# Kernel optimization log

Hardware: AMD Instinct MI355X
Metric: run time of the kernel (lower is better)

Reference implementation:

```python
import jax, jax.numpy as jnp
import numpy as np

RADIUS = [3, 3, 4, 4]
DILATION = [1, 2, 1, 2]
N_HEAD = 4
D_K = 8
SCALE = 1.0 / np.sqrt(8.0)  # module hardcodes sqrt(8)


def _patches(a, r, d):
    # a: (b, t, c, h, w) -> (b, t, c, ls2, h, w), dilated (2r+1)x(2r+1) window,
    # zero padding (invalid positions masked separately).
    b, t, c, h, w = a.shape
    p = r * d
    ap = jnp.pad(a, ((0, 0), (0, 0), (0, 0), (p, p), (p, p)))
    ls = 2 * r + 1
    sl = [ap[..., dy * d:dy * d + h, dx * d:dx * d + w]
          for dy in range(ls) for dx in range(ls)]
    return jnp.stack(sl, axis=3)


def _valid_mask(h, w, r, d):
    # (ls2, h, w) bool: True where window position is inside the image
    m = _patches(jnp.ones((1, 1, 1, h, w)), r, d)
    return m[0, 0, 0] > 0.5


def _head_attn(q, k, v, r, d):
    # q,k,v: (b, t, c, h, w); attention over all t' frames x local window
    b, t, c, h, w = q.shape
    kp = _patches(k, r, d)        # (b, t', c, p, h, w)
    vp = _patches(v, r, d)
    valid = _valid_mask(h, w, r, d)  # (p, h, w)
    e = jnp.einsum('btchw,bscphw->btsphw', q, kp) * SCALE
    e = jnp.where(valid[None, None, None], e, -jnp.inf)  # OOB -> -inf like CUDA kernel
    e = e.reshape(b, t, t * valid.shape[0], h, w)
    attn = jax.nn.softmax(e, axis=2).reshape(b, t, t, -1, h, w)
    return jnp.einsum('btsphw,bscphw->btchw', attn, vp)


def setup_inputs() -> dict:
    key = jax.random.key(0)
    kx, kq, kk, kv, ko = jax.random.split(key, 5)
    C = 32
    std = 1.0 / np.sqrt(C)
    x = jax.random.normal(kx, (2, 5, C, 64, 64), dtype=jnp.float32)
    Wq = jax.random.normal(kq, (N_HEAD * D_K, C), dtype=jnp.float32) * std
    Wk = jax.random.normal(kk, (N_HEAD * D_K, C), dtype=jnp.float32) * std
    Wv = jax.random.normal(kv, (N_HEAD * D_K, C), dtype=jnp.float32) * std
    Wo = jax.random.normal(ko, (C, C), dtype=jnp.float32) * std
    return {"x": x, "Wq": Wq, "Wk": Wk, "Wv": Wv, "Wo": Wo}


def reference(x, Wq, Wk, Wv, Wo):
    # 1x1x1 Conv3d == per-pixel channel matmul
    q = jnp.einsum('btchw,kc->btkhw', x, Wq)
    k = jnp.einsum('btchw,kc->btkhw', x, Wk)
    v = jnp.einsum('btchw,kc->btkhw', x, Wv)
    outs = []
    for i in range(N_HEAD):
        s = slice(i * D_K, (i + 1) * D_K)
        outs.append(_head_attn(q[:, :, s], k[:, :, s], v[:, :, s],
                               RADIUS[i], DILATION[i]))
    out = jnp.concatenate(outs, axis=2)
    out = jnp.einsum('btchw,kc->btkhw', out, Wo)
    return out + x
```

## Files before the change

kernel.cpp:

```cpp
#include <hip/hip_runtime.h>
#include <stdint.h>

#define NT 5
#define NC 32
#define NH 4
#define HW 4096
#define NPIX 40960
#define QS 0.51006972789f
#define EBIAS 12.0f
#define NINF (-__builtin_inff())

typedef _Float16 half_t;
typedef half_t h2 __attribute__((ext_vector_type(2)));

static __device__ __forceinline__ h2 as_h2(uint32_t u) {
  union { uint32_t u; h2 h; } c; c.u = u; return c.h;
}
static __device__ __forceinline__ uint32_t pack_h2(float a, float b) {
  union { h2 h; uint32_t u; } c;
  c.h.x = (half_t)a; c.h.y = (half_t)b;
  return c.u;
}

#if __has_builtin(__builtin_amdgcn_exp2f)
#define EXP2(x) __builtin_amdgcn_exp2f(x)
#else
#define EXP2(x) exp2f(x)
#endif

static __device__ __forceinline__ float dot8i(const uint4& a, const uint4& b, float c) {
#if __has_builtin(__builtin_amdgcn_fdot2)
  c = __builtin_amdgcn_fdot2(as_h2(a.x), as_h2(b.x), c, false);
  c = __builtin_amdgcn_fdot2(as_h2(a.y), as_h2(b.y), c, false);
  c = __builtin_amdgcn_fdot2(as_h2(a.z), as_h2(b.z), c, false);
  c = __builtin_amdgcn_fdot2(as_h2(a.w), as_h2(b.w), c, false);
  return c;
#else
  const h2 a0 = as_h2(a.x), a1 = as_h2(a.y), a2 = as_h2(a.z), a3 = as_h2(a.w);
  const h2 b0 = as_h2(b.x), b1 = as_h2(b.y), b2 = as_h2(b.z), b3 = as_h2(b.w);
  c = fmaf((float)a0.x, (float)b0.x, c);
  c = fmaf((float)a0.y, (float)b0.y, c);
  c = fmaf((float)a1.x, (float)b1.x, c);
  c = fmaf((float)a1.y, (float)b1.y, c);
  c = fmaf((float)a2.x, (float)b2.x, c);
  c = fmaf((float)a2.y, (float)b2.y, c);
  c = fmaf((float)a3.x, (float)b3.x, c);
  c = fmaf((float)a3.y, (float)b3.y, c);
  return c;
#endif
}

__global__ __launch_bounds__(256) void qkv_kernel(
    const float* __restrict__ x,
    const float* __restrict__ Wq, const float* __restrict__ Wk,
    const float* __restrict__ Wv,
    uint2* __restrict__ qf, uint2* __restrict__ kf, uint2* __restrict__ vf)
{
  const int p   = blockIdx.x * 256 + threadIdx.x;
  const int by  = blockIdx.y;
  const int h   = by >> 1;
  const int jg  = by & 1;
  const int bt  = p >> 12;
  const int pix = p & 4095;

  const float* xp = x + (size_t)bt * (NC * HW) + pix;
  float xc[NC];
  #pragma unroll
  for (int c = 0; c < NC; ++c) xc[c] = xp[(size_t)c * HW];

  float qv[4], kv4[4], vv4[4];
  #pragma unroll
  for (int j = 0; j < 4; ++j) {
    const int o = h * 8 + jg * 4 + j;
    float aq = 0.f, ak = 0.f, av = 0.f;
    #pragma unroll
    for (int c = 0; c < NC; ++c) {
      const float xv = xc[c];
      aq = fmaf(xv, Wq[o * NC + c], aq);
      ak = fmaf(xv, Wk[o * NC + c], ak);
      av = fmaf(xv, Wv[o * NC + c], av);
    }
    qv[j] = aq * QS; kv4[j] = ak; vv4[j] = av;
  }
  const size_t base = (((size_t)bt * NH + h) * HW + pix) * 2 + jg;
  uint2 qq, kk, vv;
  qq.x = pack_h2(qv[0], qv[1]);  qq.y = pack_h2(qv[2], qv[3]);
  kk.x = pack_h2(kv4[0], kv4[1]); kk.y = pack_h2(kv4[2], kv4[3]);
  vv.x = pack_h2(vv4[0], vv4[1]); vv.y = pack_h2(vv4[2], vv4[3]);
  qf[base] = qq;
  kf[base] = kk;
  vf[base] = vv;
}

template <int R, int D>
static __device__ __forceinline__ void attn_body(
    int b, int t, int h, int s, int yb,
    const uint4* __restrict__ qf, const uint4* __restrict__ kf,
    const uint4* __restrict__ vf,
    uint4* __restrict__ pa, float* __restrict__ pl,
    uint4* __restrict__ k_lds, uint4* __restrict__ v_lds)
{
  constexpr int LS    = 2 * R + 1;
  constexpr int NROWS = 8 + 2 * R;
  const int tid  = threadIdx.x;
  const int w    = tid >> 6;
  const int lane = tid & 63;

  const int y0 = (D == 1) ? (yb * 8) : ((yb & 1) + 2 * ((yb >> 1) * 8));

  const uint4* kg = kf + (size_t)((b * NT + s) * NH + h) * HW;
  const uint4* vg = vf + (size_t)((b * NT + s) * NH + h) * HW;
  for (int idx = tid; idx < NROWS * 64; idx += 256) {
    const int r  = idx >> 6, xs = idx & 63;
    int ys = y0 + (r - R) * D;
    ys = ys < 0 ? 0 : (ys > 63 ? 63 : ys);
    const int pos = (D == 1) ? xs : ((xs & 1) * 32 + (xs >> 1));
    k_lds[r * 64 + pos] = kg[ys * 64 + xs];
    v_lds[r * 64 + pos] = vg[ys * 64 + xs];
  }
  __syncthreads();

  const int xp = lane >> 5;
  const int cb = (D == 1) ? lane : (lane & 31);
  const int x  = (D == 1) ? lane : (2 * (lane & 31) + xp);
  const int yA = y0 + 2 * w * D;
  const int yB = yA + D;
  const int pixA = yA * 64 + x, pixB = yB * 64 + x;

  const uint4* qp = qf + (size_t)((b * NT + t) * NH + h) * HW;
  const uint4 qA = qp[pixA];
  const uint4 qB = qp[pixB];

  float lA = 0.f, lB = 0.f;
  h2 aA[4], aB[4];
  const h2 z2 = { (half_t)0.f, (half_t)0.f };
  #pragma unroll
  for (int i = 0; i < 4; ++i) { aA[i] = z2; aB[i] = z2; }

  #pragma unroll 2
  for (int u = 0; u <= LS; ++u) {
    const bool okA = (u < LS) && ((unsigned)(yA + (u - R) * D) < 64u);
    const bool okB = (u > 0)  && ((unsigned)(yB + (u - 1 - R) * D) < 64u);
    if (!(okA || okB)) continue;
    const float biA = okA ? -EBIAS : NINF;
    const float biB = okB ? -EBIAS : NINF;
    const uint4* kr = k_lds + (2 * w + u) * 64;
    const uint4* vr = v_lds + (2 * w + u) * 64;
    #pragma unroll
    for (int dx = -R; dx <= R; ++dx) {
      const int  cx  = cb + dx;
      const bool okx = (unsigned)cx < (D == 1 ? 64u : 32u);
      const int  cc  = okx ? cx : 0;
      const int  pos = (D == 1) ? cc : (xp * 32 + cc);
      const uint4 kk = kr[pos];
      const uint4 vv = vr[pos];
      const h2 w0 = as_h2(vv.x), w1 = as_h2(vv.y), w2 = as_h2(vv.z), w3 = as_h2(vv.w);
      const float eo = okx ? 0.f : NINF;
      const float pA = EXP2(dot8i(qA, kk, biA + eo));
      const float pB = EXP2(dot8i(qB, kk, biB + eo));
      lA += pA; lB += pB;
      const half_t pAh = (half_t)pA, pBh = (half_t)pB;
      const h2 pA2 = { pAh, pAh }, pB2 = { pBh, pBh };
      aA[0] += pA2 * w0; aA[1] += pA2 * w1; aA[2] += pA2 * w2; aA[3] += pA2 * w3;
      aB[0] += pB2 * w0; aB[1] += pB2 * w1; aB[2] += pB2 * w2; aB[3] += pB2 * w3;
    }
  }

  const size_t plane = (size_t)(s * NH + h) * NPIX + (size_t)(b * NT + t) * HW;
  union { h2 hh[4]; uint4 u; } cA, cB;
  #pragma unroll
  for (int i = 0; i < 4; ++i) { cA.hh[i] = aA[i]; cB.hh[i] = aB[i]; }
  pa[plane + pixA] = cA.u;
  pa[plane + pixB] = cB.u;
  pl[plane + pixA] = lA;
  pl[plane + pixB] = lB;
}

__global__ __launch_bounds__(256) void attn_kernel(
    const uint4* __restrict__ qf, const uint4* __restrict__ kf,
    const uint4* __restrict__ vf, uint4* __restrict__ pa, float* __restrict__ pl)
{
  __shared__ uint4 k_lds[16 * 64];
  __shared__ uint4 v_lds[16 * 64];
  const int bid = blockIdx.x;
  const int h   = bid & 3;
  int r = bid >> 2;
  const int yb = r & 7; r >>= 3;
  const int s  = r % 5;
  const int bt = r / 5;
  const int t = bt % NT, b = bt / NT;
  if      (h == 0) attn_body<3, 1>(b, t, 0, s, yb, qf, kf, vf, pa, pl, k_lds, v_lds);
  else if (h == 1) attn_body<3, 2>(b, t, 1, s, yb, qf, kf, vf, pa, pl, k_lds, v_lds);
  else if (h == 2) attn_body<4, 1>(b, t, 2, s, yb, qf, kf, vf, pa, pl, k_lds, v_lds);
  else             attn_body<4, 2>(b, t, 3, s, yb, qf, kf, vf, pa, pl, k_lds, v_lds);
}

__global__ __launch_bounds__(256) void proj_kernel(
    const uint4* __restrict__ pa, const float* __restrict__ pl,
    const float* __restrict__ x, const float* __restrict__ Wo,
    float* __restrict__ out)
{
  const int p   = blockIdx.x * 256 + threadIdx.x;
  const int og  = blockIdx.y;
  const int bt  = p >> 12;
  const int pix = p & 4095;

  float oc[32];
  #pragma unroll
  for (int h = 0; h < NH; ++h) {
    float a[8], l = 0.f;
    #pragma unroll
    for (int i = 0; i < 8; ++i) a[i] = 0.f;
    #pragma unroll
    for (int s = 0; s < NT; ++s) {
      const size_t plane = (size_t)(s * NH + h) * NPIX + p;
      const uint4 v = pa[plane];
      l += pl[plane];
      const h2 v0 = as_h2(v.x), v1 = as_h2(v.y), v2 = as_h2(v.z), v3 = as_h2(v.w);
      a[0] += (float)v0.x; a[1] += (float)v0.y;
      a[2] += (float)v1.x; a[3] += (float)v1.y;
      a[4] += (float)v2.x; a[5] += (float)v2.y;
      a[6] += (float)v3.x; a[7] += (float)v3.y;
    }
    const float inv = 1.0f / l;
    #pragma unroll
    for (int i = 0; i < 8; ++i) oc[h * 8 + i] = a[i] * inv;
  }

  const float* xpt = x + (size_t)bt * (NC * HW) + pix;
  float* yp = out + (size_t)bt * (NC * HW) + pix;
  #pragma unroll
  for (int oo = 0; oo < 8; ++oo) {
    const int o = og * 8 + oo;
    float acc = xpt[(size_t)o * HW];
    #pragma unroll
    for (int c = 0; c < NC; ++c)
      acc = fmaf(oc[c], Wo[o * NC + c], acc);
    yp[(size_t)o * HW] = acc;
  }
}

extern "C" void kernel_launch(void* const* d_in, const int* in_sizes, int n_in,
                              void* d_out, int out_size, void* d_ws, size_t ws_size,
                              hipStream_t stream)
{
  const float* x  = (const float*)d_in[0];
  const float* Wq = (const float*)d_in[1];
  const float* Wk = (const float*)d_in[2];
  const float* Wv = (const float*)d_in[3];
  const float* Wo = (const float*)d_in[4];

  char* ws = (char*)d_ws;
  uint2* qf = (uint2*)ws;
  uint2* kf = (uint2*)(ws + 2621440);
  uint2* vf = (uint2*)(ws + 2 * 2621440);
  uint4* pa = (uint4*)(ws + 3 * 2621440);
  float* pl = (float*)(ws + 3 * 2621440 + 13107200);

  qkv_kernel<<<dim3(160, 8), 256, 0, stream>>>(x, Wq, Wk, Wv, qf, kf, vf);
  attn_kernel<<<1600, 256, 0, stream>>>((const uint4*)qf, (const uint4*)kf,
                                        (const uint4*)vf, pa, pl);
  proj_kernel<<<dim3(160, 4), 256, 0, stream>>>(pa, pl, x, Wo, (float*)d_out);
}
```

Measured before the change: 117.3 us.

## Compute four query rows per wavefront to reuse each loaded K/V row

Each attention block now covers 16 output rows instead of 8. Each wavefront handles four query rows instead of two, so every K/V row read from LDS feeds up to four queries rather than two. The LDS halo overhead per output row shrinks and the grid is halved. In exchange, register pressure rises from the four accumulator sets, the LDS footprint grows, and there are fewer blocks to fill the GPU.

```diff
diff --git a/kernel.cpp b/kernel.cpp
--- a/kernel.cpp
+++ b/kernel.cpp
@@ -101,12 +101,12 @@
     uint4* __restrict__ k_lds, uint4* __restrict__ v_lds)
 {
   constexpr int LS    = 2 * R + 1;
-  constexpr int NROWS = 8 + 2 * R;
+  constexpr int NROWS = 16 + 2 * R;
   const int tid  = threadIdx.x;
   const int w    = tid >> 6;
   const int lane = tid & 63;
 
-  const int y0 = (D == 1) ? (yb * 8) : ((yb & 1) + 2 * ((yb >> 1) * 8));
+  const int y0 = (D == 1) ? (yb * 16) : ((yb & 1) + 32 * (yb >> 1));
 
   const uint4* kg = kf + (size_t)((b * NT + s) * NH + h) * HW;
   const uint4* vg = vf + (size_t)((b * NT + s) * NH + h) * HW;
@@ -123,29 +123,34 @@
   const int xp = lane >> 5;
   const int cb = (D == 1) ? lane : (lane & 31);
   const int x  = (D == 1) ? lane : (2 * (lane & 31) + xp);
-  const int yA = y0 + 2 * w * D;
-  const int yB = yA + D;
-  const int pixA = yA * 64 + x, pixB = yB * 64 + x;
+
+  int yq[4];
+  #pragma unroll
+  for (int j = 0; j < 4; ++j) yq[j] = y0 + (4 * w + j) * D;
 
   const uint4* qp = qf + (size_t)((b * NT + t) * NH + h) * HW;
-  const uint4 qA = qp[pixA];
-  const uint4 qB = qp[pixB];
-
-  float lA = 0.f, lB = 0.f;
-  h2 aA[4], aB[4];
+  uint4 q[4];
+  #pragma unroll
+  for (int j = 0; j < 4; ++j) q[j] = qp[yq[j] * 64 + x];
+
+  float l[4] = {0.f, 0.f, 0.f, 0.f};
+  h2 a[4][4];
   const h2 z2 = { (half_t)0.f, (half_t)0.f };
   #pragma unroll
-  for (int i = 0; i < 4; ++i) { aA[i] = z2; aB[i] = z2; }
-
-  #pragma unroll 2
-  for (int u = 0; u <= LS; ++u) {
-    const bool okA = (u < LS) && ((unsigned)(yA + (u - R) * D) < 64u);
-    const bool okB = (u > 0)  && ((unsigned)(yB + (u - 1 - R) * D) < 64u);
-    if (!(okA || okB)) continue;
-    const float biA = okA ? -EBIAS : NINF;
-    const float biB = okB ? -EBIAS : NINF;
-    const uint4* kr = k_lds + (2 * w + u) * 64;
-    const uint4* vr = v_lds + (2 * w + u) * 64;
+  for (int j = 0; j < 4; ++j)
+    #pragma unroll
+    for (int i = 0; i < 4; ++i) a[j][i] = z2;
+
+  #pragma unroll 1
+  for (int u = 0; u < 2 * R + 4; ++u) {
+    const int yk = y0 + (4 * w + u - R) * D;
+    if ((unsigned)yk >= 64u) continue;
+    float bi[4];
+    #pragma unroll
+    for (int j = 0; j < 4; ++j)
+      bi[j] = ((unsigned)(u - j) <= (unsigned)(2 * R)) ? -EBIAS : NINF;
+    const uint4* kr = k_lds + (4 * w + u) * 64;
+    const uint4* vr = v_lds + (4 * w + u) * 64;
     #pragma unroll
     for (int dx = -R; dx <= R; ++dx) {
       const int  cx  = cb + dx;
@@ -156,36 +161,40 @@
       const uint4 vv = vr[pos];
       const h2 w0 = as_h2(vv.x), w1 = as_h2(vv.y), w2 = as_h2(vv.z), w3 = as_h2(vv.w);
       const float eo = okx ? 0.f : NINF;
-      const float pA = EXP2(dot8i(qA, kk, biA + eo));
-      const float pB = EXP2(dot8i(qB, kk, biB + eo));
-      lA += pA; lB += pB;
-      const half_t pAh = (half_t)pA, pBh = (half_t)pB;
-      const h2 pA2 = { pAh, pAh }, pB2 = { pBh, pBh };
-      aA[0] += pA2 * w0; aA[1] += pA2 * w1; aA[2] += pA2 * w2; aA[3] += pA2 * w3;
-      aB[0] += pB2 * w0; aB[1] += pB2 * w1; aB[2] += pB2 * w2; aB[3] += pB2 * w3;
+      #pragma unroll
+      for (int j = 0; j < 4; ++j) {
+        const float p = EXP2(dot8i(q[j], kk, bi[j] + eo));
+        l[j] += p;
+        const half_t ph = (half_t)p;
+        const h2 p2 = { ph, ph };
+        a[j][0] += p2 * w0; a[j][1] += p2 * w1;
+        a[j][2] += p2 * w2; a[j][3] += p2 * w3;
+      }
     }
   }
 
   const size_t plane = (size_t)(s * NH + h) * NPIX + (size_t)(b * NT + t) * HW;
-  union { h2 hh[4]; uint4 u; } cA, cB;
-  #pragma unroll
-  for (int i = 0; i < 4; ++i) { cA.hh[i] = aA[i]; cB.hh[i] = aB[i]; }
-  pa[plane + pixA] = cA.u;
-  pa[plane + pixB] = cB.u;
-  pl[plane + pixA] = lA;
-  pl[plane + pixB] = lB;
+  #pragma unroll
+  for (int j = 0; j < 4; ++j) {
+    union { h2 hh[4]; uint4 u; } c;
+    #pragma unroll
+    for (int i = 0; i < 4; ++i) c.hh[i] = a[j][i];
+    const int pix = yq[j] * 64 + x;
+    pa[plane + pix] = c.u;
+    pl[plane + pix] = l[j];
+  }
 }
 
 __global__ __launch_bounds__(256) void attn_kernel(
     const uint4* __restrict__ qf, const uint4* __restrict__ kf,
     const uint4* __restrict__ vf, uint4* __restrict__ pa, float* __restrict__ pl)
 {
-  __shared__ uint4 k_lds[16 * 64];
-  __shared__ uint4 v_lds[16 * 64];
+  __shared__ uint4 k_lds[24 * 64];
+  __shared__ uint4 v_lds[24 * 64];
   const int bid = blockIdx.x;
   const int h   = bid & 3;
   int r = bid >> 2;
-  const int yb = r & 7; r >>= 3;
+  const int yb = r & 3; r >>= 2;
   const int s  = r % 5;
   const int bt = r / 5;
   const int t = bt % NT, b = bt / NT;
@@ -258,7 +267,7 @@
   float* pl = (float*)(ws + 3 * 2621440 + 13107200);
 
   qkv_kernel<<<dim3(160, 8), 256, 0, stream>>>(x, Wq, Wk, Wv, qf, kf, vf);
-  attn_kernel<<<1600, 256, 0, stream>>>((const uint4*)qf, (const uint4*)kf,
-                                        (const uint4*)vf, pa, pl);
+  attn_kernel<<<800, 256, 0, stream>>>((const uint4*)qf, (const uint4*)kf,
+                                       (const uint4*)vf, pa, pl);
   proj_kernel<<<dim3(160, 4), 256, 0, stream>>>(pa, pl, x, Wo, (float*)d_out);
 }
```

Result: slower. 127.6 us (+8.8%).
